# Performance work log

Measured on AMD Instinct MI355X. Metric: run time of the kernel, lower is better.

## Reference

```python
import jax, jax.numpy as jnp
import numpy as np

B, L, D_MODEL = 2, 2048, 512
EXPAND, D_STATE, D_CONV = 2, 16, 4
D_INNER = EXPAND * D_MODEL          # 1024
DT_RANK = (D_MODEL + 15) // 16      # 32
HIDDEN = 2048
LN_EPS = 1e-5


def setup_inputs() -> dict:
    key = jax.random.key(0)
    ks = iter(jax.random.split(key, 64))
    rn = lambda shape, s=0.02: jax.random.normal(next(ks), shape, jnp.float32) * s
    inp = {}
    inp["x"] = jax.random.normal(next(ks), (B, L, D_MODEL), jnp.float32)
    inp["ln1_w"] = jnp.ones((D_MODEL,), jnp.float32)
    inp["ln1_b"] = jnp.zeros((D_MODEL,), jnp.float32)
    inp["in_proj_w"] = rn((2 * D_INNER, D_MODEL))
    A_init = jnp.log(jnp.tile(jnp.arange(1, D_STATE + 1, dtype=jnp.float32), (D_INNER, 1)))
    dt_bias0 = float(np.log(np.expm1(0.01)))  # mamba-style dt bias init (~-4.6)
    for sfx in ["", "_b"]:
        inp["conv_w" + sfx] = rn((D_INNER, 1, D_CONV), 0.1)
        inp["conv_b" + sfx] = jnp.zeros((D_INNER,), jnp.float32)
        inp["x_proj_w" + sfx] = rn((DT_RANK + 2 * D_STATE, D_INNER))
        inp["dt_proj_w" + sfx] = rn((D_INNER, DT_RANK), 0.1)
        inp["dt_proj_b" + sfx] = rn((D_INNER,), 0.1) + dt_bias0
        inp["A_log" + sfx] = A_init
        inp["D_param" + sfx] = jnp.ones((D_INNER,), jnp.float32)
    inp["out_proj_w"] = rn((D_MODEL, D_INNER))
    inp["ln2_w"] = jnp.ones((D_MODEL,), jnp.float32)
    inp["ln2_b"] = jnp.zeros((D_MODEL,), jnp.float32)
    inp["fc1_w"] = rn((HIDDEN, D_MODEL))
    inp["fc1_b"] = jnp.zeros((HIDDEN,), jnp.float32)
    inp["fc2_w"] = rn((D_MODEL, HIDDEN))
    inp["fc2_b"] = jnp.zeros((D_MODEL,), jnp.float32)
    return inp


def _layernorm(x, w, b):
    m = x.mean(-1, keepdims=True)
    v = ((x - m) ** 2).mean(-1, keepdims=True)
    return (x - m) * jax.lax.rsqrt(v + LN_EPS) * w + b


def _silu(x):
    return x * jax.nn.sigmoid(x)


def _mamba_dir(xz, conv_w, conv_b, x_proj_w, dt_proj_w, dt_proj_b, A_log, Dp):
    # xz: [B, 2*d_inner, L] (channel-first, one scan direction)
    u, z = jnp.split(xz, 2, axis=1)
    # depthwise causal conv, kernel 4, left pad 3 -> same length L
    u = jax.lax.conv_general_dilated(u, conv_w, (1,), [(D_CONV - 1, 0)],
                                     dimension_numbers=("NCH", "OIH", "NCH"),
                                     feature_group_count=D_INNER) + conv_b[None, :, None]
    u = _silu(u)
    ut = u.transpose(0, 2, 1)                       # [B, L, d_inner]
    x_dbl = ut @ x_proj_w.T                          # [B, L, dt_rank + 2N]
    dt, Bm, Cm = jnp.split(x_dbl, [DT_RANK, DT_RANK + D_STATE], axis=-1)
    dt = jax.nn.softplus(dt @ dt_proj_w.T + dt_proj_b)  # [B, L, d_inner]
    A = -jnp.exp(A_log)                              # [d_inner, N]

    def step(h, xs):
        dt_t, B_t, C_t, u_t = xs                     # [B,d],[B,N],[B,N],[B,d]
        dA = jnp.exp(dt_t[..., None] * A)            # [B, d, N]
        h = dA * h + (dt_t * u_t)[..., None] * B_t[:, None, :]
        y_t = jnp.einsum("bdn,bn->bd", h, C_t)
        return h, y_t

    h0 = jnp.zeros((ut.shape[0], D_INNER, D_STATE), ut.dtype)
    xs = (dt.transpose(1, 0, 2), Bm.transpose(1, 0, 2), Cm.transpose(1, 0, 2), ut.transpose(1, 0, 2))
    _, ys = jax.lax.scan(step, h0, xs)               # ys: [L, B, d_inner]
    y = ys.transpose(1, 0, 2) + ut * Dp              # skip term D*u
    return y * _silu(z.transpose(0, 2, 1))           # gated, [B, L, d_inner]


def reference(x, ln1_w, ln1_b, in_proj_w,
              conv_w, conv_b, x_proj_w, dt_proj_w, dt_proj_b, A_log, D_param,
              conv_w_b, conv_b_b, x_proj_w_b, dt_proj_w_b, dt_proj_b_b, A_log_b, D_param_b,
              out_proj_w, ln2_w, ln2_b, fc1_w, fc1_b, fc2_w, fc2_b):
    # --- Mamba branch (bimamba v2, if_divide_out=True) ---
    xn = _layernorm(x, ln1_w, ln1_b)
    xz = jnp.einsum("bld,ed->bel", xn, in_proj_w)    # [B, 2*d_inner, L]
    y_f = _mamba_dir(xz, conv_w, conv_b, x_proj_w, dt_proj_w, dt_proj_b, A_log, D_param)
    y_b = _mamba_dir(jnp.flip(xz, axis=-1), conv_w_b, conv_b_b, x_proj_w_b,
                     dt_proj_w_b, dt_proj_b_b, A_log_b, D_param_b)
    y = (y_f + jnp.flip(y_b, axis=1)) * 0.5          # if_divide_out
    x = x + y @ out_proj_w.T
    # --- MLP branch ---
    x2 = _layernorm(x, ln2_w, ln2_b)
    h = jax.nn.gelu(x2 @ fc1_w.T + fc1_b, approximate=False)
    x = x + (h @ fc2_w.T + fc2_b)
    return x
```

## Files before the change

### kernel.cpp

```cpp
#include <hip/hip_runtime.h>
#include <hip/hip_bf16.h>


#define B_   2
#define L_   2048
#define DM   512
#define DI   1024
#define E2   2048
#define NS   16
#define HID  2048
#define ROWS (B_ * L_)
#define CH   32
#define TT   (L_ / CH)
#define NCH  4096

typedef __bf16 bf16_t;
typedef bf16_t bf16x8 __attribute__((ext_vector_type(8)));
typedef float f32x4 __attribute__((ext_vector_type(4)));
typedef unsigned int u32;
typedef unsigned short u16;

__device__ __forceinline__ float fexp2(float x) { return __builtin_amdgcn_exp2f(x); }
__device__ __forceinline__ float fexp(float x)  { return fexp2(x * 1.44269504f); }
__device__ __forceinline__ float frcp(float x)  { return __builtin_amdgcn_rcpf(x); }
__device__ __forceinline__ float sigm(float x)  { return frcp(1.f + fexp2(-1.44269504f * x)); }

template<int PAT>
__device__ __forceinline__ float swzadd(float q)
{
    return q + __int_as_float(__builtin_amdgcn_ds_swizzle(__float_as_int(q), PAT));
}

__device__ __forceinline__ u16 f2bu(float f)
{
    __hip_bfloat16 h = __float2bfloat16(f);
    return *(u16*)&h;
}

__global__ __launch_bounds__(64)
void ln_kernel(const float* __restrict__ in, const float* __restrict__ w,
               const float* __restrict__ b, __hip_bfloat16* __restrict__ out)
{
    const int row  = blockIdx.x;
    const int lane = threadIdx.x;
    const float* p = in + (size_t)row * DM;
    float v[8];
    float s = 0.f;
#pragma unroll
    for (int i = 0; i < 8; ++i) { v[i] = p[lane + 64 * i]; s += v[i]; }
#pragma unroll
    for (int off = 32; off > 0; off >>= 1) s += __shfl_xor(s, off);
    const float mean = s * (1.f / DM);
    float vs = 0.f;
#pragma unroll
    for (int i = 0; i < 8; ++i) { float d = v[i] - mean; vs += d * d; }
#pragma unroll
    for (int off = 32; off > 0; off >>= 1) vs += __shfl_xor(vs, off);
    const float rstd = rsqrtf(vs * (1.f / DM) + 1e-5f);
    __hip_bfloat16* o = out + (size_t)row * DM;
#pragma unroll
    for (int i = 0; i < 8; ++i) {
        const int c = lane + 64 * i;
        o[c] = __float2bfloat16((v[i] - mean) * rstd * w[c] + b[c]);
    }
}

template<int MODE, int OUT, int SPLITK>
__global__ __launch_bounds__(256)
void mgemm(const __hip_bfloat16* __restrict__ A, int lda,
           const __hip_bfloat16* __restrict__ W, int ldw,
           const float* __restrict__ bias,
           const float* __restrict__ res, int ldres,
           void* __restrict__ Cptr, int ldc,
           int M, int K)
{
    __shared__ __align__(16) bf16_t lsA[128 * 32];
    __shared__ __align__(16) bf16_t lsB[128 * 32];

    const int bm = blockIdx.y * 128;
    const int bn = blockIdx.x * 128;
    const int kLen = K / SPLITK;
    const int kBeg = blockIdx.z * kLen;

    const int t = threadIdx.x;
    const int l = t & 63, wid = t >> 6;
    const int wr = wid >> 1, wc = wid & 1;
    const int lrow = l & 15, lk = l >> 4;
    const int xorf = (lrow >> 1) & 3;
    const int rdoff = (lk ^ xorf) * 8;

    const int r0 = t >> 2,          c0 = t & 3;
    const int r1 = (256 + t) >> 2,  c1 = t & 3;
    const int sc0 = c0 ^ ((r0 >> 1) & 3);
    const int sc1 = c1 ^ ((r1 >> 1) & 3);

    const bf16_t* gA0 = (const bf16_t*)A + (size_t)(bm + r0) * lda + kBeg + sc0 * 8;
    const bf16_t* gA1 = (const bf16_t*)A + (size_t)(bm + r1) * lda + kBeg + sc1 * 8;
    const bf16_t* gB0 = (const bf16_t*)W + (size_t)(bn + r0) * ldw + kBeg + sc0 * 8;
    const bf16_t* gB1 = (const bf16_t*)W + (size_t)(bn + r1) * ldw + kBeg + sc1 * 8;
    bf16_t* dA0 = &lsA[(size_t)t * 8];
    bf16_t* dA1 = &lsA[(size_t)(256 + t) * 8];
    bf16_t* dB0 = &lsB[(size_t)t * 8];
    bf16_t* dB1 = &lsB[(size_t)(256 + t) * 8];

    f32x4 acc[4][4] = {};

    for (int k0 = 0; k0 < kLen; k0 += 32) {
        __builtin_amdgcn_global_load_lds(
            (const __attribute__((address_space(1))) void*)gA0,
            (__attribute__((address_space(3))) void*)dA0, 16, 0, 0);
        __builtin_amdgcn_global_load_lds(
            (const __attribute__((address_space(1))) void*)gA1,
            (__attribute__((address_space(3))) void*)dA1, 16, 0, 0);
        __builtin_amdgcn_global_load_lds(
            (const __attribute__((address_space(1))) void*)gB0,
            (__attribute__((address_space(3))) void*)dB0, 16, 0, 0);
        __builtin_amdgcn_global_load_lds(
            (const __attribute__((address_space(1))) void*)gB1,
            (__attribute__((address_space(3))) void*)dB1, 16, 0, 0);
        gA0 += 32; gA1 += 32; gB0 += 32; gB1 += 32;
        __syncthreads();

        bf16x8 af[4], bfv[4];
#pragma unroll
        for (int m = 0; m < 4; ++m) {
            const int ra = wr * 64 + m * 16 + lrow;
            af[m] = *(const bf16x8*)&lsA[ra * 32 + rdoff];
        }
#pragma unroll
        for (int n = 0; n < 4; ++n) {
            const int rb = wc * 64 + n * 16 + lrow;
            bfv[n] = *(const bf16x8*)&lsB[rb * 32 + rdoff];
        }
#pragma unroll
        for (int m = 0; m < 4; ++m)
#pragma unroll
            for (int n = 0; n < 4; ++n)
                acc[m][n] = __builtin_amdgcn_mfma_f32_16x16x32_bf16(
                    af[m], bfv[n], acc[m][n], 0, 0, 0);
        __syncthreads();
    }

    float* Cf = (float*)Cptr;
    __hip_bfloat16* Cb = (__hip_bfloat16*)Cptr;
    if (OUT == 2) Cf += (size_t)blockIdx.z * M * ldc;

#pragma unroll
    for (int m = 0; m < 4; ++m) {
#pragma unroll
        for (int n = 0; n < 4; ++n) {
#pragma unroll
            for (int j = 0; j < 4; ++j) {
                const int row = bm + wr * 64 + m * 16 + lk * 4 + j;
                const int col = bn + wc * 64 + n * 16 + lrow;
                float v = acc[m][n][j];
                if (MODE == 1) {
                    v += bias[col];
                    v = (v > 20.f) ? v
                        : 0.69314718f * __builtin_amdgcn_logf(1.f + fexp2(1.44269504f * v));
                } else if (MODE == 3) {
                    v += bias[col];
                    v = 0.5f * v * (1.f + erff(v * 0.70710678118654752f));
                }
                if (OUT == 1) Cb[(size_t)row * ldc + col] = __float2bfloat16(v);
                else          Cf[(size_t)row * ldc + col] = v;
            }
        }
    }
}

__global__ __launch_bounds__(256)
void k_prep(const float* __restrict__ ipw, const float* __restrict__ f1w,
            const float* __restrict__ f2w,
            const float* __restrict__ xpf, const float* __restrict__ xpb,
            const float* __restrict__ dwf, const float* __restrict__ dwb,
            const float* __restrict__ dbf, const float* __restrict__ dbb,
            const float* __restrict__ wo,
            __hip_bfloat16* __restrict__ wip, __hip_bfloat16* __restrict__ wfc1,
            __hip_bfloat16* __restrict__ wfc2, __hip_bfloat16* __restrict__ wxp,
            __hip_bfloat16* __restrict__ wdt, __hip_bfloat16* __restrict__ wop,
            float* __restrict__ dtbias)
{
    const int bid = blockIdx.x;
    const int tid = threadIdx.x;
    if (bid < 4096) {
        const int i = bid * 256 + tid;
        wip[i] = __float2bfloat16(ipw[i]);
    } else if (bid < 8192) {
        const int i = (bid - 4096) * 256 + tid;
        wfc1[i] = __float2bfloat16(f1w[i]);
    } else if (bid < 12288) {
        const int i = (bid - 8192) * 256 + tid;
        wfc2[i] = __float2bfloat16(f2w[i]);
    } else if (bid < 13312) {
        const int idx = (bid - 12288) * 256 + tid;
        const int r = idx >> 11, c = idx & 2047;
        float v = 0.f;
        if (r < 64) { if (c < 1024) v = xpf[r * 1024 + c]; }
        else        { if (c >= 1024) v = xpb[(r - 64) * 1024 + (c - 1024)]; }
        wxp[idx] = __float2bfloat16(v);
    } else if (bid < 14336) {
        const int idx = (bid - 13312) * 256 + tid;
        const int r = idx >> 7, c = idx & 127;
        float v = 0.f;
        if (r < 1024) { if (c < 32) v = dwf[r * 32 + c]; }
        else          { if (c >= 64 && c < 96) v = dwb[(r - 1024) * 32 + (c - 64)]; }
        wdt[idx] = __float2bfloat16(v);
        if (idx < 2048) dtbias[idx] = (idx < 1024) ? dbf[idx] : dbb[idx - 1024];
    } else {
        const int idx = (bid - 14336) * 256 + tid;
        const int r = idx >> 11, c = idx & 2047;
        wop[idx] = __float2bfloat16(0.5f * wo[r * 1024 + (c & 1023)]);
    }
}

__global__ __launch_bounds__(256)
void conv2_kernel(const __hip_bfloat16* __restrict__ xz,
                  const float* __restrict__ wf, const float* __restrict__ bf_,
                  const float* __restrict__ wb, const float* __restrict__ bb_,
                  __hip_bfloat16* __restrict__ out)
{
    const int idx = blockIdx.x * 256 + threadIdx.x;
    const int e = idx & 2047;
    const int dir = e >> 10;
    const int d = e & 1023;
    const int t = (idx >> 11) & (L_ - 1);
    const int b = idx >> 22;
    const __hip_bfloat16* base = xz + (size_t)b * L_ * E2 + d;
    const float* w = dir ? wb : wf;
    float acc = dir ? bb_[d] : bf_[d];
#pragma unroll
    for (int k = 0; k < 4; ++k) {
        const int tt = dir ? (t + 3 - k) : (t - 3 + k);
        if (tt >= 0 && tt < L_)
            acc += w[d * 4 + k] * __bfloat162float(base[(size_t)tt * E2]);
    }
    out[idx] = __float2bfloat16(acc * sigm(acc));
}

__global__ void k_red2(const float* __restrict__ part,
                       __hip_bfloat16* __restrict__ xb,
                       float* __restrict__ sB4, float* __restrict__ sC4)
{
    const int idx = blockIdx.x * 256 + threadIdx.x;
    float s4 = 0.f;
#pragma unroll
    for (int z = 0; z < 8; ++z) s4 += part[idx + z * 524288];
    xb[idx] = __float2bfloat16(s4);
    const int col = idx & 127, row = idx >> 7;
    const int c64 = col & 63, dirq = col >> 6;
    if (c64 >= 32) {
        const int bq = row >> 11, tt = row & 2047;
        const int s = dirq ? (L_ - 1 - tt) : tt;
        const int n = c64 & 15;
        const int g = dirq * 2 + bq;
        float* dst = (c64 < 48 ? sB4 : sC4) + ((size_t)g * L_ + s) * 16 + n;
        *dst = s4;
    }
}

__global__ __launch_bounds__(256)
void k_scanprep(const __hip_bfloat16* __restrict__ dtb,
                const __hip_bfloat16* __restrict__ ucv,
                u32* __restrict__ sdtdu)
{
    __shared__ u32 lds[32][65];
    const int bid = blockIdx.x;
    const int st  = bid & 63;
    const int dtl = (bid >> 6) & 15;
    const int b   = (bid >> 10) & 1;
    const int dir = bid >> 11;
    const int tid = threadIdx.x;
    {
        const int r = tid >> 3, c8 = (tid & 7) * 8;
        const int s = st * 32 + r;
        const int tt = dir ? (L_ - 1 - s) : s;
        const size_t row = (size_t)b * L_ + tt;
        const int e = dir * 1024 + dtl * 64 + c8;
        const uint4 dv = *(const uint4*)((const u16*)dtb + row * E2 + e);
        const uint4 uv = *(const uint4*)((const u16*)ucv + row * E2 + e);
        const u32 dw[4] = { dv.x, dv.y, dv.z, dv.w };
        const u32 uw[4] = { uv.x, uv.y, uv.z, uv.w };
#pragma unroll
        for (int j = 0; j < 4; ++j) {
            lds[r][c8 + 2 * j]     = ((uw[j] & 0xffffu) << 16) | (dw[j] & 0xffffu);
            lds[r][c8 + 2 * j + 1] = (uw[j] & 0xffff0000u) | (dw[j] >> 16);
        }
    }
    __syncthreads();
    {
        const int cd = tid >> 2, s8 = (tid & 3) * 8;
        const int chain = dir * 2048 + b * 1024 + dtl * 64 + cd;
        u32* dst = sdtdu + (size_t)chain * L_ + st * 32 + s8;
#pragma unroll
        for (int j = 0; j < 8; ++j) dst[j] = lds[s8 + j][cd];
    }
}

__global__ __launch_bounds__(256)
void scan_p1(const u32* __restrict__ sdtdu, const float* __restrict__ sB4,
             const float* __restrict__ AlF, const float* __restrict__ AlB,
             float* __restrict__ P, float* __restrict__ Hend)
{
    const int tid = threadIdx.x;
    const int j = tid & 3;
    const int task = blockIdx.x * 64 + (tid >> 2);
    const int chain = task & (NCH - 1);
    const int c = task >> 12;
    const int dir = chain >> 11;
    const int b = (chain >> 10) & 1;
    const int d = chain & 1023;
    const int g = dir * 2 + b;

    const float* Al = dir ? AlB : AlF;
    const float4 al = *(const float4*)(Al + d * NS + j * 4);
    const float An2[4] = { -fexp(al.x) * 1.44269504f, -fexp(al.y) * 1.44269504f,
                           -fexp(al.z) * 1.44269504f, -fexp(al.w) * 1.44269504f };

    const u32* pdt = sdtdu + (size_t)chain * L_ + c * TT;
    const float* pB = sB4 + ((size_t)g * L_ + c * TT) * 16 + j * 4;

    float h[4] = { 0.f, 0.f, 0.f, 0.f };
    float sdt = 0.f;
    for (int i = 0; i < TT; i += 4) {
        const uint4 pk = *(const uint4*)(pdt + i);
        const u32 wv[4] = { pk.x, pk.y, pk.z, pk.w };
#pragma unroll
        for (int k = 0; k < 4; ++k) {
            const float dt = __uint_as_float(wv[k] << 16);
            const float uu = __uint_as_float(wv[k] & 0xffff0000u);
            const float w = dt * uu;
            const float4 B4 = *(const float4*)(pB + (i + k) * 16);
            h[0] = fexp2(dt * An2[0]) * h[0] + w * B4.x;
            h[1] = fexp2(dt * An2[1]) * h[1] + w * B4.y;
            h[2] = fexp2(dt * An2[2]) * h[2] + w * B4.z;
            h[3] = fexp2(dt * An2[3]) * h[3] + w * B4.w;
            sdt += dt;
        }
    }
    float4 Pv = { fexp2(An2[0] * sdt), fexp2(An2[1] * sdt),
                  fexp2(An2[2] * sdt), fexp2(An2[3] * sdt) };
    *(float4*)(P + (size_t)task * NS + j * 4) = Pv;
    float4 Hv = { h[0], h[1], h[2], h[3] };
    *(float4*)(Hend + (size_t)task * NS + j * 4) = Hv;
}

__global__ __launch_bounds__(256)
void scan_p2(const float* __restrict__ P, float* __restrict__ Hend)
{
    const int tid = threadIdx.x;
    const int n = tid & 15;
    const int chain = blockIdx.x * 16 + (tid >> 4);
    float hin = 0.f;
    for (int c = 0; c < CH; ++c) {
        const size_t idx = ((size_t)c * NCH + chain) * NS + n;
        const float nh = P[idx] * hin + Hend[idx];
        Hend[idx] = hin;
        hin = nh;
    }
}

__global__ __launch_bounds__(256)
void scan_p3(const u32* __restrict__ sdtdu, const float* __restrict__ sB4,
             const float* __restrict__ sC4,
             const float* __restrict__ AlF, const float* __restrict__ AlB,
             const float* __restrict__ DpF, const float* __restrict__ DpB,
             const float* __restrict__ Hin,
             const __hip_bfloat16* __restrict__ xz,
             __hip_bfloat16* __restrict__ yall)
{
    __shared__ u16 ly[64][68];
    const int tid = threadIdx.x;
    const int j = tid & 3;
    const int task = blockIdx.x * 64 + (tid >> 2);
    const int chain = task & (NCH - 1);
    const int c = task >> 12;
    const int dir = chain >> 11;
    const int b = (chain >> 10) & 1;
    const int d = chain & 1023;
    const int g = dir * 2 + b;

    const float* Al = dir ? AlB : AlF;
    const float4 al = *(const float4*)(Al + d * NS + j * 4);
    const float An2[4] = { -fexp(al.x) * 1.44269504f, -fexp(al.y) * 1.44269504f,
                           -fexp(al.z) * 1.44269504f, -fexp(al.w) * 1.44269504f };
    const float Dd = (dir ? DpB : DpF)[d];

    const u32* pdt = sdtdu + (size_t)chain * L_ + c * TT;
    const float* pB = sB4 + ((size_t)g * L_ + c * TT) * 16 + j * 4;
    const float* pC = sC4 + ((size_t)g * L_ + c * TT) * 16 + j * 4;

    const float4 hv = *(const float4*)(Hin + (size_t)task * NS + j * 4);
    float h[4] = { hv.x, hv.y, hv.z, hv.w };

    for (int i = 0; i < TT; i += 4) {
        const uint4 pk = *(const uint4*)(pdt + i);
        const u32 wv[4] = { pk.x, pk.y, pk.z, pk.w };
        float qv[4], us[4];
#pragma unroll
        for (int k = 0; k < 4; ++k) {
            const float dt = __uint_as_float(wv[k] << 16);
            const float uu = __uint_as_float(wv[k] & 0xffff0000u);
            us[k] = uu;
            const float w = dt * uu;
            const float4 B4 = *(const float4*)(pB + (i + k) * 16);
            const float4 C4 = *(const float4*)(pC + (i + k) * 16);
            h[0] = fexp2(dt * An2[0]) * h[0] + w * B4.x;
            h[1] = fexp2(dt * An2[1]) * h[1] + w * B4.y;
            h[2] = fexp2(dt * An2[2]) * h[2] + w * B4.z;
            h[3] = fexp2(dt * An2[3]) * h[3] + w * B4.w;
            qv[k] = h[0] * C4.x + h[1] * C4.y + h[2] * C4.z + h[3] * C4.w;
        }
#pragma unroll
        for (int k = 0; k < 4; ++k) qv[k] = swzadd<0x041F>(qv[k]);
#pragma unroll
        for (int k = 0; k < 4; ++k) qv[k] = swzadd<0x081F>(qv[k]);
        if (j == 0) {
            uint2 pkd;
            pkd.x = (u32)f2bu(qv[0] + us[0] * Dd) | ((u32)f2bu(qv[1] + us[1] * Dd) << 16);
            pkd.y = (u32)f2bu(qv[2] + us[2] * Dd) | ((u32)f2bu(qv[3] + us[3] * Dd) << 16);
            *(uint2*)&ly[tid >> 2][i] = pkd;
        }
    }
    __syncthreads();

    {
        const int cb = (blockIdx.x * 64) & (NCH - 1);
        const int dir2 = cb >> 11, b2 = (cb >> 10) & 1, dbase = cb & 1023;
        const int c2 = (blockIdx.x * 64) >> 12;
        const int sl = tid >> 2;
        const int dql = (tid & 3) * 16;
        const int s = c2 * TT + sl;
        const int tt = dir2 ? (L_ - 1 - s) : s;
        const size_t row = (size_t)b2 * L_ + tt;
        const u16* zp = (const u16*)xz + row * E2 + 1024 + dbase + dql;
        const uint4 zv0 = *(const uint4*)zp;
        const uint4 zv1 = *(const uint4*)(zp + 8);
        const u32 zw[8] = { zv0.x, zv0.y, zv0.z, zv0.w, zv1.x, zv1.y, zv1.z, zv1.w };
        u16 ov[16];
#pragma unroll
        for (int jj = 0; jj < 8; ++jj) {
            const float z0 = __uint_as_float(zw[jj] << 16);
            const float z1 = __uint_as_float(zw[jj] & 0xffff0000u);
            const float y0 = __uint_as_float((u32)ly[dql + 2 * jj][sl] << 16);
            const float y1 = __uint_as_float((u32)ly[dql + 2 * jj + 1][sl] << 16);
            ov[2 * jj]     = f2bu(y0 * (z0 * sigm(z0)));
            ov[2 * jj + 1] = f2bu(y1 * (z1 * sigm(z1)));
        }
        u16* op = (u16*)yall + row * E2 + dir2 * 1024 + dbase + dql;
        *(uint4*)op = *(uint4*)ov;
        *(uint4*)(op + 8) = *(uint4*)(ov + 8);
    }
}

__global__ __launch_bounds__(256)
void k_redln(const float* __restrict__ part, const float* __restrict__ x,
             const float* __restrict__ w, const float* __restrict__ bb,
             float* __restrict__ xmid, __hip_bfloat16* __restrict__ xn2)
{
    const int row = blockIdx.x * 4 + (threadIdx.x >> 6);
    const int lane = threadIdx.x & 63;
    const size_t base = (size_t)row * DM;
    const int c0 = lane * 4, c1 = 256 + lane * 4;

    const float4 p0a = *(const float4*)(part + base + c0);
    const float4 p1a = *(const float4*)(part + 2097152 + base + c0);
    const float4 xa  = *(const float4*)(x + base + c0);
    const float4 p0b = *(const float4*)(part + base + c1);
    const float4 p1b = *(const float4*)(part + 2097152 + base + c1);
    const float4 xb  = *(const float4*)(x + base + c1);
    float v[8];
    v[0] = xa.x + p0a.x + p1a.x; v[1] = xa.y + p0a.y + p1a.y;
    v[2] = xa.z + p0a.z + p1a.z; v[3] = xa.w + p0a.w + p1a.w;
    v[4] = xb.x + p0b.x + p1b.x; v[5] = xb.y + p0b.y + p1b.y;
    v[6] = xb.z + p0b.z + p1b.z; v[7] = xb.w + p0b.w + p1b.w;
    float4 oa = { v[0], v[1], v[2], v[3] }, ob = { v[4], v[5], v[6], v[7] };
    *(float4*)(xmid + base + c0) = oa;
    *(float4*)(xmid + base + c1) = ob;

    float s = 0.f;
#pragma unroll
    for (int i = 0; i < 8; ++i) s += v[i];
#pragma unroll
    for (int off = 32; off > 0; off >>= 1) s += __shfl_xor(s, off);
    const float mean = s * (1.f / DM);
    float vs = 0.f;
#pragma unroll
    for (int i = 0; i < 8; ++i) { float dd = v[i] - mean; vs += dd * dd; }
#pragma unroll
    for (int off = 32; off > 0; off >>= 1) vs += __shfl_xor(vs, off);
    const float rstd = rsqrtf(vs * (1.f / DM) + 1e-5f);

    u16 o0[4], o1[4];
#pragma unroll
    for (int i = 0; i < 4; ++i) {
        o0[i] = f2bu((v[i] - mean) * rstd * w[c0 + i] + bb[c0 + i]);
        o1[i] = f2bu((v[4 + i] - mean) * rstd * w[c1 + i] + bb[c1 + i]);
    }
    *(uint2*)((u16*)xn2 + base + c0) = *(uint2*)o0;
    *(uint2*)((u16*)xn2 + base + c1) = *(uint2*)o1;
}

__global__ __launch_bounds__(256)
void k_redfc2(const float* __restrict__ part, const float* __restrict__ res,
              const float* __restrict__ bias, float* __restrict__ out)
{
    const int i = (blockIdx.x * 256 + threadIdx.x) * 4;
    const int col = i & (DM - 1);
    const float4 p0 = *(const float4*)(part + i);
    const float4 p1 = *(const float4*)(part + 2097152 + i);
    const float4 rv = *(const float4*)(res + i);
    const float4 bv = *(const float4*)(bias + col);
    float4 o;
    o.x = rv.x + bv.x + p0.x + p1.x; o.y = rv.y + bv.y + p0.y + p1.y;
    o.z = rv.z + bv.z + p0.z + p1.z; o.w = rv.w + bv.w + p0.w + p1.w;
    *(float4*)(out + i) = o;
}

extern "C" void kernel_launch(void* const* d_in, const int* in_sizes, int n_in,
                              void* d_out, int out_size, void* d_ws, size_t ws_size,
                              hipStream_t stream)
{
    const float* x         = (const float*)d_in[0];
    const float* ln1_w     = (const float*)d_in[1];
    const float* ln1_b     = (const float*)d_in[2];
    const float* in_proj_w = (const float*)d_in[3];
    const float* conv_w[2]    = { (const float*)d_in[4],  (const float*)d_in[11] };
    const float* conv_b[2]    = { (const float*)d_in[5],  (const float*)d_in[12] };
    const float* x_proj_w[2]  = { (const float*)d_in[6],  (const float*)d_in[13] };
    const float* dt_proj_w[2] = { (const float*)d_in[7],  (const float*)d_in[14] };
    const float* dt_proj_b[2] = { (const float*)d_in[8],  (const float*)d_in[15] };
    const float* A_log[2]     = { (const float*)d_in[9],  (const float*)d_in[16] };
    const float* D_param[2]   = { (const float*)d_in[10], (const float*)d_in[17] };
    const float* out_proj_w = (const float*)d_in[18];
    const float* ln2_w      = (const float*)d_in[19];
    const float* ln2_b      = (const float*)d_in[20];
    const float* fc1_w      = (const float*)d_in[21];
    const float* fc1_b      = (const float*)d_in[22];
    const float* fc2_w      = (const float*)d_in[23];
    const float* fc2_b      = (const float*)d_in[24];
    float* out = (float*)d_out;

    char* ws = (char*)d_ws;
    const size_t MB = 1u << 20;
    __hip_bfloat16* wip  = (__hip_bfloat16*)(ws + 0 * MB);
    __hip_bfloat16* wxp  = (__hip_bfloat16*)(ws + 2 * MB);
    __hip_bfloat16* wdt  = (__hip_bfloat16*)(ws + 2 * MB + 512 * 1024);
    __hip_bfloat16* wop  = (__hip_bfloat16*)(ws + 3 * MB);
    __hip_bfloat16* wfc1 = (__hip_bfloat16*)(ws + 5 * MB);
    __hip_bfloat16* wfc2 = (__hip_bfloat16*)(ws + 7 * MB);
    float* dtbias        = (float*)(ws + 9 * MB);
    __hip_bfloat16* xz   = (__hip_bfloat16*)(ws + 10 * MB);
    __hip_bfloat16* ucv  = (__hip_bfloat16*)(ws + 26 * MB);
    float* Ps            = (float*)(ws + 26 * MB);
    float* Hend          = (float*)(ws + 34 * MB);
    __hip_bfloat16* dtb  = (__hip_bfloat16*)(ws + 42 * MB);
    float* xdbp          = (float*)(ws + 58 * MB);
    __hip_bfloat16* xn1  = (__hip_bfloat16*)(ws + 74 * MB);
    __hip_bfloat16* xdbb = (__hip_bfloat16*)(ws + 78 * MB);
    u32* sdtdu           = (u32*)(ws + 58 * MB);
    float* part          = (float*)(ws + 58 * MB);
    __hip_bfloat16* yall = (__hip_bfloat16*)(ws + 90 * MB);
    float* sB4           = (float*)(ws + 106 * MB);
    float* sC4           = (float*)(ws + 106 * MB + 512 * 1024);
    float* xmid          = (float*)(ws + 10 * MB);
    __hip_bfloat16* xn2  = (__hip_bfloat16*)(ws + 18 * MB);
    __hip_bfloat16* h1   = (__hip_bfloat16*)(ws + 26 * MB);

    k_prep<<<18432, 256, 0, stream>>>(
        in_proj_w, fc1_w, fc2_w, x_proj_w[0], x_proj_w[1],
        dt_proj_w[0], dt_proj_w[1], dt_proj_b[0], dt_proj_b[1], out_proj_w,
        wip, wfc1, wfc2, wxp, wdt, wop, dtbias);

    ln_kernel<<<ROWS, 64, 0, stream>>>(x, ln1_w, ln1_b, xn1);

    mgemm<0, 1, 1><<<dim3(16, 32, 1), 256, 0, stream>>>(
        xn1, DM, wip, DM, nullptr, nullptr, 0, xz, E2, ROWS, DM);

    conv2_kernel<<<(B_ * L_ * E2) / 256, 256, 0, stream>>>(
        xz, conv_w[0], conv_b[0], conv_w[1], conv_b[1], ucv);

    mgemm<0, 2, 8><<<dim3(1, 32, 8), 256, 0, stream>>>(
        ucv, E2, wxp, E2, nullptr, nullptr, 0, xdbp, 128, ROWS, E2);
    k_red2<<<2048, 256, 0, stream>>>(xdbp, xdbb, sB4, sC4);

    mgemm<1, 1, 1><<<dim3(16, 32, 1), 256, 0, stream>>>(
        xdbb, 128, wdt, 128, dtbias, nullptr, 0, dtb, E2, ROWS, 128);

    k_scanprep<<<4096, 256, 0, stream>>>(dtb, ucv, sdtdu);

    scan_p1<<<(CH * NCH) / 64, 256, 0, stream>>>(
        sdtdu, sB4, A_log[0], A_log[1], Ps, Hend);
    scan_p2<<<NCH / 16, 256, 0, stream>>>(Ps, Hend);
    scan_p3<<<(CH * NCH) / 64, 256, 0, stream>>>(
        sdtdu, sB4, sC4, A_log[0], A_log[1], D_param[0], D_param[1],
        Hend, xz, yall);

    mgemm<0, 2, 2><<<dim3(4, 32, 2), 256, 0, stream>>>(
        yall, E2, wop, E2, nullptr, nullptr, 0, part, DM, ROWS, E2);
    k_redln<<<1024, 256, 0, stream>>>(part, x, ln2_w, ln2_b, xmid, xn2);

    mgemm<3, 1, 1><<<dim3(16, 32, 1), 256, 0, stream>>>(
        xn2, DM, wfc1, DM, fc1_b, nullptr, 0, h1, HID, ROWS, DM);

    mgemm<0, 2, 2><<<dim3(4, 32, 2), 256, 0, stream>>>(
        h1, HID, wfc2, HID, nullptr, nullptr, 0, part, DM, ROWS, HID);
    k_redfc2<<<2048, 256, 0, stream>>>(part, xmid, fc2_b, out);
}
```

Measured before the change: 280.4 us.

## Fuse scan prep transpose with first scan pass using LDS-resident dt/u

Merges k_scanprep and scan_p1 into one kernel. Each block transposes a 64-step tile of packed dt/u into LDS, writes it out for scan_p3, and then runs the chunk-local scan directly from LDS, so the global re-read of sdtdu in pass 1 and one kernel launch go away. Workspace buffers are reassigned so the fused kernel's outputs do not alias its inputs, and the LDS padding and store width in scan_p3 are adjusted. The chunk count implied by st is now 32 steps of 64, which matches CH, but the per-block LDS use grows and the transpose writes are column-strided.

```diff
diff --git a/kernel.cpp b/kernel.cpp
--- a/kernel.cpp
+++ b/kernel.cpp
@@ -260,89 +260,91 @@
 }
 
 __global__ __launch_bounds__(256)
-void k_scanprep(const __hip_bfloat16* __restrict__ dtb,
+void k_scanscan(const __hip_bfloat16* __restrict__ dtb,
                 const __hip_bfloat16* __restrict__ ucv,
-                u32* __restrict__ sdtdu)
-{
-    __shared__ u32 lds[32][65];
+                const float* __restrict__ sB4,
+                const float* __restrict__ AlF, const float* __restrict__ AlB,
+                u32* __restrict__ sdtdu,
+                float* __restrict__ P, float* __restrict__ Hend)
+{
+    __shared__ u32 lds[64][65];
     const int bid = blockIdx.x;
-    const int st  = bid & 63;
-    const int dtl = (bid >> 6) & 15;
-    const int b   = (bid >> 10) & 1;
-    const int dir = bid >> 11;
+    const int st  = bid & 31;
+    const int dtl = (bid >> 5) & 15;
+    const int b   = (bid >> 9) & 1;
+    const int dir = bid >> 10;
     const int tid = threadIdx.x;
+    const int g = dir * 2 + b;
+
     {
-        const int r = tid >> 3, c8 = (tid & 7) * 8;
-        const int s = st * 32 + r;
-        const int tt = dir ? (L_ - 1 - s) : s;
-        const size_t row = (size_t)b * L_ + tt;
-        const int e = dir * 1024 + dtl * 64 + c8;
-        const uint4 dv = *(const uint4*)((const u16*)dtb + row * E2 + e);
-        const uint4 uv = *(const uint4*)((const u16*)ucv + row * E2 + e);
-        const u32 dw[4] = { dv.x, dv.y, dv.z, dv.w };
-        const u32 uw[4] = { uv.x, uv.y, uv.z, uv.w };
-#pragma unroll
-        for (int j = 0; j < 4; ++j) {
-            lds[r][c8 + 2 * j]     = ((uw[j] & 0xffffu) << 16) | (dw[j] & 0xffffu);
-            lds[r][c8 + 2 * j + 1] = (uw[j] & 0xffff0000u) | (dw[j] >> 16);
+        const int c8 = (tid & 7) * 8;
+#pragma unroll
+        for (int rr = 0; rr < 2; ++rr) {
+            const int r = (tid >> 3) + rr * 32;
+            const int s = st * 64 + r;
+            const int tt = dir ? (L_ - 1 - s) : s;
+            const size_t row = (size_t)b * L_ + tt;
+            const int e = dir * 1024 + dtl * 64 + c8;
+            const uint4 dv = *(const uint4*)((const u16*)dtb + row * E2 + e);
+            const uint4 uv = *(const uint4*)((const u16*)ucv + row * E2 + e);
+            const u32 dw[4] = { dv.x, dv.y, dv.z, dv.w };
+            const u32 uw[4] = { uv.x, uv.y, uv.z, uv.w };
+#pragma unroll
+            for (int jj = 0; jj < 4; ++jj) {
+                lds[c8 + 2 * jj][r]     = ((uw[jj] & 0xffffu) << 16) | (dw[jj] & 0xffffu);
+                lds[c8 + 2 * jj + 1][r] = (uw[jj] & 0xffff0000u) | (dw[jj] >> 16);
+            }
         }
     }
     __syncthreads();
+
     {
-        const int cd = tid >> 2, s8 = (tid & 3) * 8;
+        const int cd = tid >> 2, s16 = (tid & 3) * 16;
         const int chain = dir * 2048 + b * 1024 + dtl * 64 + cd;
-        u32* dst = sdtdu + (size_t)chain * L_ + st * 32 + s8;
-#pragma unroll
-        for (int j = 0; j < 8; ++j) dst[j] = lds[s8 + j][cd];
-    }
-}
-
-__global__ __launch_bounds__(256)
-void scan_p1(const u32* __restrict__ sdtdu, const float* __restrict__ sB4,
-             const float* __restrict__ AlF, const float* __restrict__ AlB,
-             float* __restrict__ P, float* __restrict__ Hend)
-{
-    const int tid = threadIdx.x;
-    const int j = tid & 3;
-    const int task = blockIdx.x * 64 + (tid >> 2);
-    const int chain = task & (NCH - 1);
-    const int c = task >> 12;
-    const int dir = chain >> 11;
-    const int b = (chain >> 10) & 1;
-    const int d = chain & 1023;
-    const int g = dir * 2 + b;
-
-    const float* Al = dir ? AlB : AlF;
-    const float4 al = *(const float4*)(Al + d * NS + j * 4);
-    const float An2[4] = { -fexp(al.x) * 1.44269504f, -fexp(al.y) * 1.44269504f,
-                           -fexp(al.z) * 1.44269504f, -fexp(al.w) * 1.44269504f };
-
-    const u32* pdt = sdtdu + (size_t)chain * L_ + c * TT;
-    const float* pB = sB4 + ((size_t)g * L_ + c * TT) * 16 + j * 4;
-
-    float h[4] = { 0.f, 0.f, 0.f, 0.f };
-    float sdt = 0.f;
-    for (int i = 0; i < TT; i += 4) {
-        const uint4 pk = *(const uint4*)(pdt + i);
-        const u32 wv[4] = { pk.x, pk.y, pk.z, pk.w };
-#pragma unroll
-        for (int k = 0; k < 4; ++k) {
-            const float dt = __uint_as_float(wv[k] << 16);
-            const float uu = __uint_as_float(wv[k] & 0xffff0000u);
+        u32* dst = sdtdu + (size_t)chain * L_ + st * 64 + s16;
+#pragma unroll
+        for (int jj = 0; jj < 4; ++jj) {
+            uint4 v;
+            v.x = lds[cd][s16 + 4 * jj + 0];
+            v.y = lds[cd][s16 + 4 * jj + 1];
+            v.z = lds[cd][s16 + 4 * jj + 2];
+            v.w = lds[cd][s16 + 4 * jj + 3];
+            *(uint4*)(dst + 4 * jj) = v;
+        }
+    }
+
+    {
+        const int j = tid & 3;
+        const int cd = tid >> 2;
+        const int chain = dir * 2048 + b * 1024 + dtl * 64 + cd;
+        const int d = chain & 1023;
+        const float* Al = dir ? AlB : AlF;
+        const float4 al = *(const float4*)(Al + d * NS + j * 4);
+        const float An2[4] = { -fexp(al.x) * 1.44269504f, -fexp(al.y) * 1.44269504f,
+                               -fexp(al.z) * 1.44269504f, -fexp(al.w) * 1.44269504f };
+        const float* pB = sB4 + ((size_t)g * L_ + st * 64) * 16 + j * 4;
+
+        float h[4] = { 0.f, 0.f, 0.f, 0.f };
+        float sdt = 0.f;
+        for (int i = 0; i < 64; ++i) {
+            const u32 w32 = lds[cd][i];
+            const float dt = __uint_as_float(w32 << 16);
+            const float uu = __uint_as_float(w32 & 0xffff0000u);
             const float w = dt * uu;
-            const float4 B4 = *(const float4*)(pB + (i + k) * 16);
+            const float4 B4 = *(const float4*)(pB + i * 16);
             h[0] = fexp2(dt * An2[0]) * h[0] + w * B4.x;
             h[1] = fexp2(dt * An2[1]) * h[1] + w * B4.y;
             h[2] = fexp2(dt * An2[2]) * h[2] + w * B4.z;
             h[3] = fexp2(dt * An2[3]) * h[3] + w * B4.w;
             sdt += dt;
         }
-    }
-    float4 Pv = { fexp2(An2[0] * sdt), fexp2(An2[1] * sdt),
-                  fexp2(An2[2] * sdt), fexp2(An2[3] * sdt) };
-    *(float4*)(P + (size_t)task * NS + j * 4) = Pv;
-    float4 Hv = { h[0], h[1], h[2], h[3] };
-    *(float4*)(Hend + (size_t)task * NS + j * 4) = Hv;
+        const int task = st * NCH + chain;
+        float4 Pv = { fexp2(An2[0] * sdt), fexp2(An2[1] * sdt),
+                      fexp2(An2[2] * sdt), fexp2(An2[3] * sdt) };
+        *(float4*)(P + (size_t)task * NS + j * 4) = Pv;
+        float4 Hv = { h[0], h[1], h[2], h[3] };
+        *(float4*)(Hend + (size_t)task * NS + j * 4) = Hv;
+    }
 }
 
 __global__ __launch_bounds__(256)
@@ -369,7 +371,7 @@
              const __hip_bfloat16* __restrict__ xz,
              __hip_bfloat16* __restrict__ yall)
 {
-    __shared__ u16 ly[64][68];
+    __shared__ u16 ly[64][70];
     const int tid = threadIdx.x;
     const int j = tid & 3;
     const int task = blockIdx.x * 64 + (tid >> 2);
@@ -416,10 +418,9 @@
 #pragma unroll
         for (int k = 0; k < 4; ++k) qv[k] = swzadd<0x081F>(qv[k]);
         if (j == 0) {
-            uint2 pkd;
-            pkd.x = (u32)f2bu(qv[0] + us[0] * Dd) | ((u32)f2bu(qv[1] + us[1] * Dd) << 16);
-            pkd.y = (u32)f2bu(qv[2] + us[2] * Dd) | ((u32)f2bu(qv[3] + us[3] * Dd) << 16);
-            *(uint2*)&ly[tid >> 2][i] = pkd;
+            u32* lp = (u32*)&ly[tid >> 2][i];
+            lp[0] = (u32)f2bu(qv[0] + us[0] * Dd) | ((u32)f2bu(qv[1] + us[1] * Dd) << 16);
+            lp[1] = (u32)f2bu(qv[2] + us[2] * Dd) | ((u32)f2bu(qv[3] + us[3] * Dd) << 16);
         }
     }
     __syncthreads();
@@ -552,20 +553,20 @@
     float* dtbias        = (float*)(ws + 9 * MB);
     __hip_bfloat16* xz   = (__hip_bfloat16*)(ws + 10 * MB);
     __hip_bfloat16* ucv  = (__hip_bfloat16*)(ws + 26 * MB);
-    float* Ps            = (float*)(ws + 26 * MB);
-    float* Hend          = (float*)(ws + 34 * MB);
     __hip_bfloat16* dtb  = (__hip_bfloat16*)(ws + 42 * MB);
     float* xdbp          = (float*)(ws + 58 * MB);
+    float* Ps            = (float*)(ws + 58 * MB);
+    float* Hend          = (float*)(ws + 66 * MB);
     __hip_bfloat16* xn1  = (__hip_bfloat16*)(ws + 74 * MB);
     __hip_bfloat16* xdbb = (__hip_bfloat16*)(ws + 78 * MB);
-    u32* sdtdu           = (u32*)(ws + 58 * MB);
-    float* part          = (float*)(ws + 58 * MB);
-    __hip_bfloat16* yall = (__hip_bfloat16*)(ws + 90 * MB);
+    u32* sdtdu           = (u32*)(ws + 74 * MB);
+    float* part          = (float*)(ws + 74 * MB);
+    __hip_bfloat16* yall = (__hip_bfloat16*)(ws + 26 * MB);
     float* sB4           = (float*)(ws + 106 * MB);
     float* sC4           = (float*)(ws + 106 * MB + 512 * 1024);
     float* xmid          = (float*)(ws + 10 * MB);
     __hip_bfloat16* xn2  = (__hip_bfloat16*)(ws + 18 * MB);
-    __hip_bfloat16* h1   = (__hip_bfloat16*)(ws + 26 * MB);
+    __hip_bfloat16* h1   = (__hip_bfloat16*)(ws + 42 * MB);
 
     k_prep<<<18432, 256, 0, stream>>>(
         in_proj_w, fc1_w, fc2_w, x_proj_w[0], x_proj_w[1],
@@ -587,10 +588,8 @@
     mgemm<1, 1, 1><<<dim3(16, 32, 1), 256, 0, stream>>>(
         xdbb, 128, wdt, 128, dtbias, nullptr, 0, dtb, E2, ROWS, 128);
 
-    k_scanprep<<<4096, 256, 0, stream>>>(dtb, ucv, sdtdu);
-
-    scan_p1<<<(CH * NCH) / 64, 256, 0, stream>>>(
-        sdtdu, sB4, A_log[0], A_log[1], Ps, Hend);
+    k_scanscan<<<2048, 256, 0, stream>>>(
+        dtb, ucv, sB4, A_log[0], A_log[1], sdtdu, Ps, Hend);
     scan_p2<<<NCH / 16, 256, 0, stream>>>(Ps, Hend);
     scan_p3<<<(CH * NCH) / 64, 256, 0, stream>>>(
         sdtdu, sB4, sC4, A_log[0], A_log[1], D_param[0], D_param[1],
```

After: 272.9 us. 2.7% less time.
